# Kernel tuning notes

Measured on AMD Instinct MI355X. Metric: run time of the kernel, lower is better.

## Reference

```python
import jax, jax.numpy as jnp
import numpy as np
from jax import lax

A, T, B, OBS, H, ACT = 4, 128, 256, 128, 128, 8  # agents, time, envs, obs_dim, gru_hidden(=embed), act_dim


def setup_inputs() -> dict:
    key = jax.random.key(0)
    ks = jax.random.split(key, 16)
    def w(k, shape, fan_in):
        return (jax.random.normal(k, shape, jnp.float32) / np.float32(np.sqrt(fan_in)))
    return {
        "hstate": jnp.zeros((A, B, H), jnp.float32),
        "obs": jax.random.normal(ks[0], (A, T, B, OBS), jnp.float32),
        "avail_actions": jnp.ones((A, T, B, ACT), jnp.float32),
        # embedding dense
        "We": w(ks[1], (A, OBS, H), OBS), "be": jnp.zeros((A, H), jnp.float32),
        # GRU: input kernels (r|z|n concat) with bias, hidden kernels (r|z|n), only n-hidden has bias
        "Wi": w(ks[2], (A, H, 3 * H), H), "bi": jnp.zeros((A, 3 * H), jnp.float32),
        "Wh": w(ks[3], (A, H, 3 * H), H), "bhn": jnp.zeros((A, H), jnp.float32),
        # actor head
        "Wa1": w(ks[4], (A, H, H), H), "ba1": jnp.zeros((A, H), jnp.float32),
        "Wa2": 0.01 * w(ks[5], (A, H, ACT), H), "ba2": jnp.zeros((A, ACT), jnp.float32),
        "log_std": jnp.zeros((A, ACT), jnp.float32),
        # critic head
        "Wc1": w(ks[6], (A, H, H), H), "bc1": jnp.zeros((A, H), jnp.float32),
        "Wc2": w(ks[7], (A, H, 1), H), "bc2": jnp.zeros((A, 1), jnp.float32),
        "done": jax.random.bernoulli(ks[8], 0.05, (A, T, B)),
    }


def _agent_forward(h0, obs, done, avail_actions, We, be, Wi, bi, Wh, bhn,
                   Wa1, ba1, Wa2, ba2, log_std, Wc1, bc1, Wc2, bc2):
    # obs: [T,B,OBS], done: [T,B], h0: [B,H]
    act = jnp.tanh  # config['network']['activation'] == 'tanh'
    emb = act(jnp.einsum('tbo,oh->tbh', obs, We) + be)          # [T,B,H]
    xi = jnp.einsum('tbh,hg->tbg', emb, Wi) + bi                # [T,B,3H] precomputed input gates

    def step(h, xs):
        xi_t, d = xs                                            # [B,3H], [B]
        h = jnp.where(d[:, None], 0.0, h)                       # reset on done
        hh = h @ Wh                                             # [B,3H]
        xr, xz, xn = jnp.split(xi_t, 3, axis=-1)
        hr, hz, hn = jnp.split(hh, 3, axis=-1)
        r = jax.nn.sigmoid(xr + hr)
        z = jax.nn.sigmoid(xz + hz)
        n = jnp.tanh(xn + r * (hn + bhn))
        h_new = (1.0 - z) * n + z * h
        return h_new, h_new

    hT, ys = lax.scan(step, h0, (xi, done))                     # ys: [T,B,H]
    a = act(jnp.einsum('tbh,hk->tbk', ys, Wa1) + ba1)
    mean = jnp.einsum('tbh,ha->tba', a, Wa2) + ba2              # [T,B,ACT]
    std = jnp.exp(log_std)                                      # [ACT]
    c = act(jnp.einsum('tbh,hk->tbk', ys, Wc1) + bc1)
    value = (jnp.einsum('tbh,ho->tbo', c, Wc2) + bc2)[..., 0]   # [T,B]
    return hT, mean, std, value


def reference(hstate, obs, avail_actions, We, be, Wi, bi, Wh, bhn,
              Wa1, ba1, Wa2, ba2, log_std, Wc1, bc1, Wc2, bc2, done):
    hT, mean, std, value = jax.vmap(_agent_forward)(
        hstate, obs, done, avail_actions, We, be, Wi, bi, Wh, bhn,
        Wa1, ba1, Wa2, ba2, log_std, Wc1, bc1, Wc2, bc2)
    return hT, mean, std, value
```

## Files before the change

kernel.cpp:

```cpp
#include <hip/hip_runtime.h>

typedef unsigned short u16;
typedef __attribute__((ext_vector_type(8))) short short8;
typedef __attribute__((ext_vector_type(4))) float f32x4;

#define A_ 4
#define T_ 128
#define B_ 256
#define OBS_ 128
#define H_ 128
#define G_ 384
#define ACT_ 8
#define SIGS -1.4426950408889634f
#define TANS 2.8853900817779268f

__device__ __forceinline__ u16 f2b(float x) {
    unsigned int u = __float_as_uint(x);
    u = (u + 0x7fffu + ((u >> 16) & 1u)) >> 16;
    return (u16)u;
}
__device__ __forceinline__ u16 f2bc(float x) {
    return (u16)((__float_as_uint(x) + 0x8000u) >> 16);
}
__device__ __forceinline__ float b2f(u16 h) {
    return __uint_as_float(((unsigned int)h) << 16);
}
__device__ __forceinline__ float fexp2_(float x) { return __builtin_amdgcn_exp2f(x); }
__device__ __forceinline__ float frcp_(float x) { return __builtin_amdgcn_rcpf(x); }
__device__ __forceinline__ float sig_pre(float x) { return frcp_(1.0f + fexp2_(x)); }
__device__ __forceinline__ float tanh_pre(float x) {
    return fmaf(-2.0f, frcp_(1.0f + fexp2_(x)), 1.0f);
}
__device__ __forceinline__ f32x4 mfma16(short8 a, short8 b, f32x4 c) {
    return __builtin_amdgcn_mfma_f32_16x16x32_bf16(a, b, c, 0, 0, 0);
}

__global__ void k_prep(const float* __restrict__ We, const float* __restrict__ Wi,
                       const float* __restrict__ Wh, const float* __restrict__ Wa1,
                       const float* __restrict__ Wc1, const float* __restrict__ Wa2,
                       const float* __restrict__ Wc2, const float* __restrict__ log_std,
                       u16* __restrict__ weT, u16* __restrict__ wiT, u16* __restrict__ whT,
                       u16* __restrict__ wa1T, u16* __restrict__ wc1T, u16* __restrict__ h2T,
                       float* __restrict__ std_out) {
    const int PER_A = 149504;
    int idx = blockIdx.x * 256 + threadIdx.x;
    const int total = 4 * PER_A;
    if (idx < total) {
        int a = idx / PER_A;
        int i = idx % PER_A;
        if (i < 16384) {
            int h = i >> 7, o = i & 127;
            weT[a * 16384 + i] = f2b(TANS * We[a * 16384 + o * 128 + h]);
        } else if (i < 16384 + 49152) {
            int j = i - 16384; int g = j >> 7, k = j & 127;
            float s = (g < 256) ? SIGS : TANS;
            wiT[a * 49152 + j] = f2b(s * Wi[a * 49152 + k * 384 + g]);
        } else if (i < 16384 + 2 * 49152) {
            int j = i - 16384 - 49152; int g = j >> 7, k = j & 127;
            float s = (g < 256) ? SIGS : TANS;
            whT[a * 49152 + j] = f2b(s * Wh[a * 49152 + k * 384 + g]);
        } else if (i < 2 * 16384 + 2 * 49152) {
            int j = i - 16384 - 2 * 49152; int h2 = j >> 7, k = j & 127;
            wa1T[a * 16384 + j] = f2b(TANS * Wa1[a * 16384 + k * 128 + h2]);
        } else if (i < 3 * 16384 + 2 * 49152) {
            int j = i - 2 * 16384 - 2 * 49152; int h2 = j >> 7, k = j & 127;
            wc1T[a * 16384 + j] = f2b(TANS * Wc1[a * 16384 + k * 128 + h2]);
        } else {
            int j = i - 3 * 16384 - 2 * 49152; int row = j >> 7, k = j & 127;
            float v = 0.f;
            if (row < 8) v = Wa2[a * 1024 + k * 8 + row];
            else if (row == 8) v = Wc2[a * 128 + k];
            h2T[a * 2048 + j] = f2b(v);
        }
    } else if (idx < total + 32) {
        int i = idx - total;
        std_out[i] = __expf(log_std[i]);
    }
}

__global__ __launch_bounds__(512) void k_embed_xi(
    const float* __restrict__ obs, const float* __restrict__ be, const float* __restrict__ bi,
    const u16* __restrict__ weT, const u16* __restrict__ wiT, u16* __restrict__ xi_ws) {
    __shared__ __align__(16) u16 obsl[2][16][136];
    __shared__ __align__(16) u16 elds[2][16][136];
    const int a = blockIdx.y, t = blockIdx.x, half = blockIdx.z;
    const int wid = threadIdx.x >> 6, lane = threadIdx.x & 63;
    const int m = lane & 15, quad = lane >> 4;
    const int srow = threadIdx.x >> 5, schunk = threadIdx.x & 31;

    short8 we[4], wi[3][4];
    {
        const u16* p = weT + a * 16384 + (wid * 16 + m) * 128 + quad * 8;
#pragma unroll
        for (int ks = 0; ks < 4; ++ks) we[ks] = *(const short8*)(p + ks * 32);
#pragma unroll
        for (int g = 0; g < 3; ++g) {
            const u16* q = wiT + a * 49152 + (g * 128 + wid * 16 + m) * 128 + quad * 8;
#pragma unroll
            for (int ks = 0; ks < 4; ++ks) wi[g][ks] = *(const short8*)(q + ks * 32);
        }
    }
    const float bee = TANS * be[a * H_ + wid * 16 + m];
    float big[3];
#pragma unroll
    for (int g = 0; g < 3; ++g)
        big[g] = ((g < 2) ? SIGS : TANS) * bi[a * G_ + g * 128 + wid * 16 + m];

    const float* obsrow = obs + ((size_t)(a * T_ + t) * B_ + half * 128 + srow) * OBS_ + schunk * 4;
    ushort4* xi4 = (ushort4*)xi_ws;

    {
        float4 p0 = *(const float4*)(obsrow);
        ushort4 ob;
        ob.x = f2b(p0.x); ob.y = f2b(p0.y); ob.z = f2b(p0.z); ob.w = f2b(p0.w);
        *(ushort4*)&obsl[0][srow][schunk * 4] = ob;
    }
    float4 pf = *(const float4*)(obsrow + 2048);
    __syncthreads();

    for (int it = 0; it < 8; ++it) {
        short8 af[4];
#pragma unroll
        for (int ks = 0; ks < 4; ++ks)
            af[ks] = *(const short8*)&obsl[it & 1][m][ks * 32 + quad * 8];
        if (it + 1 < 8) {
            ushort4 ob;
            ob.x = f2b(pf.x); ob.y = f2b(pf.y); ob.z = f2b(pf.z); ob.w = f2b(pf.w);
            *(ushort4*)&obsl[(it + 1) & 1][srow][schunk * 4] = ob;
            if (it + 2 < 8) pf = *(const float4*)(obsrow + (size_t)(it + 2) * 2048);
        }

        f32x4 acc = f32x4{bee, bee, bee, bee};
#pragma unroll
        for (int ks = 0; ks < 4; ++ks) acc = mfma16(af[ks], we[ks], acc);
#pragma unroll
        for (int r = 0; r < 4; ++r)
            elds[it & 1][quad * 4 + r][wid * 16 + m] = f2bc(tanh_pre(acc[r]));

        if (it > 0) {
            short8 ef[4];
#pragma unroll
            for (int ks = 0; ks < 4; ++ks)
                ef[ks] = *(const short8*)&elds[(it - 1) & 1][m][ks * 32 + quad * 8];
            f32x4 xa[3];
#pragma unroll
            for (int g = 0; g < 3; ++g) xa[g] = f32x4{big[g], big[g], big[g], big[g]};
#pragma unroll
            for (int ks = 0; ks < 4; ++ks)
#pragma unroll
                for (int g = 0; g < 3; ++g) xa[g] = mfma16(ef[ks], wi[g][ks], xa[g]);
            const int itg = half * 8 + it - 1;
            const size_t base = ((size_t)(a * 16 + itg) * T_ + t) * 1536;
#pragma unroll
            for (int g = 0; g < 3; ++g) {
                ushort4 pk;
                pk.x = f2bc(xa[g][0]); pk.y = f2bc(xa[g][1]);
                pk.z = f2bc(xa[g][2]); pk.w = f2bc(xa[g][3]);
                xi4[base + (size_t)(wid * 3 + g) * 64 + lane] = pk;
            }
        }
        __syncthreads();
    }
    {
        short8 ef[4];
#pragma unroll
        for (int ks = 0; ks < 4; ++ks)
            ef[ks] = *(const short8*)&elds[1][m][ks * 32 + quad * 8];
        f32x4 xa[3];
#pragma unroll
        for (int g = 0; g < 3; ++g) xa[g] = f32x4{big[g], big[g], big[g], big[g]};
#pragma unroll
        for (int ks = 0; ks < 4; ++ks)
#pragma unroll
            for (int g = 0; g < 3; ++g) xa[g] = mfma16(ef[ks], wi[g][ks], xa[g]);
        const int itg = half * 8 + 7;
        const size_t base = ((size_t)(a * 16 + itg) * T_ + t) * 1536;
#pragma unroll
        for (int g = 0; g < 3; ++g) {
            ushort4 pk;
            pk.x = f2bc(xa[g][0]); pk.y = f2bc(xa[g][1]);
            pk.z = f2bc(xa[g][2]); pk.w = f2bc(xa[g][3]);
            xi4[base + (size_t)(wid * 3 + g) * 64 + lane] = pk;
        }
    }
}

__global__ __launch_bounds__(512, 2) void k_scan(
    const float* __restrict__ hstate, const u16* __restrict__ xi_ws,
    const u16* __restrict__ whT, const float* __restrict__ bhn,
    const int* __restrict__ done,
    const u16* __restrict__ wa1T, const u16* __restrict__ wc1T, const u16* __restrict__ h2T,
    const float* __restrict__ ba1, const float* __restrict__ bc1,
    const float* __restrict__ ba2, const float* __restrict__ bc2,
    float* __restrict__ hT_out, float* __restrict__ mean_out, float* __restrict__ val_out) {
    __shared__ __align__(16) u16 hlds[2][16][136];
    __shared__ __align__(16) u16 al[2][2][16][136];
    const int a = blockIdx.y, btile = blockIdx.x;
    const int wid = threadIdx.x >> 6, lane = threadIdx.x & 63;
    const int m = lane & 15, quad = lane >> 4;
    const int b0 = btile * 16;
    const int col = 16 * wid + m;

    short8 wh[3][4];
    const u16* whTa = whT + a * 49152;
#pragma unroll
    for (int g = 0; g < 3; ++g) {
        const u16* p = whTa + (g * 128 + col) * 128 + quad * 8;
#pragma unroll
        for (int ks = 0; ks < 4; ++ks) wh[g][ks] = *(const short8*)(p + ks * 32);
    }
    short8 wa[4], wc[4], h2f[4];
    {
        const u16* pa = wa1T + a * 16384 + col * 128 + quad * 8;
        const u16* pc = wc1T + a * 16384 + col * 128 + quad * 8;
        const u16* ph = h2T + a * 2048 + m * 128 + quad * 8;
#pragma unroll
        for (int ks = 0; ks < 4; ++ks) {
            wa[ks] = *(const short8*)(pa + ks * 32);
            wc[ks] = *(const short8*)(pc + ks * 32);
            h2f[ks] = *(const short8*)(ph + ks * 32);
        }
    }
    const float bh = TANS * bhn[a * H_ + col];
    const float fa = TANS * ba1[a * 128 + col];
    const float fc = TANS * bc1[a * 128 + col];
    float bb2 = 0.f;
    if (wid == 0) { if (m < 8) bb2 = ba2[a * 8 + m]; }
    else if (wid == 1) { if (m == 8) bb2 = bc2[a]; }

    float hm[4]; u16 hb[4];
#pragma unroll
    for (int r = 0; r < 4; ++r) {
        float v = hstate[((size_t)a * B_ + b0 + quad * 4 + r) * H_ + col];
        hm[r] = v; hb[r] = f2b(v);
    }

    const ushort4* xi4 = (const ushort4*)xi_ws;
    const size_t xibase = ((size_t)(a * 16 + btile) * T_) * 1536 + wid * 192 + lane;
    const int* dptr = done + (size_t)a * T_ * B_ + b0 + quad * 4;
    const int* dAq = done + (size_t)a * T_ * B_ + b0 + m;

    ushort4 px0 = xi4[xibase], px1 = xi4[xibase + 64], px2 = xi4[xibase + 128];
    int4 dn = *(const int4*)(dptr);
    int dead = dAq[0];

    for (int t = 0; t < T_; ++t) {
        u16 (*hl)[136] = hlds[t & 1];
#pragma unroll
        for (int r = 0; r < 4; ++r) hl[quad * 4 + r][col] = hb[r];
        if (dn.x) hm[0] = 0.f;
        if (dn.y) hm[1] = 0.f;
        if (dn.z) hm[2] = 0.f;
        if (dn.w) hm[3] = 0.f;
        __syncthreads();

        f32x4 ar, az, an;
        float xn[4];
        ar[0] = b2f(px0.x); ar[1] = b2f(px0.y); ar[2] = b2f(px0.z); ar[3] = b2f(px0.w);
        az[0] = b2f(px1.x); az[1] = b2f(px1.y); az[2] = b2f(px1.z); az[3] = b2f(px1.w);
        xn[0] = b2f(px2.x); xn[1] = b2f(px2.y); xn[2] = b2f(px2.z); xn[3] = b2f(px2.w);
        an = f32x4{bh, bh, bh, bh};
        const int deadcur = dead;
        if (t + 1 < T_) {
            const size_t nx = xibase + (size_t)(t + 1) * 1536;
            px0 = xi4[nx]; px1 = xi4[nx + 64]; px2 = xi4[nx + 128];
            dn = *(const int4*)(dptr + (size_t)(t + 1) * B_);
            dead = dAq[(size_t)(t + 1) * B_];
        }

        short8 af[4];
#pragma unroll
        for (int ks = 0; ks < 4; ++ks)
            af[ks] = *(const short8*)&hl[m][ks * 32 + quad * 8];

        f32x4 aa, ac;
        if (t > 0) {
            aa = f32x4{fa, fa, fa, fa};
            ac = f32x4{fc, fc, fc, fc};
#pragma unroll
            for (int ks = 0; ks < 4; ++ks) {
                aa = mfma16(af[ks], wa[ks], aa);
                ac = mfma16(af[ks], wc[ks], ac);
            }
        }

        short8 afr[4];
#pragma unroll
        for (int ks = 0; ks < 4; ++ks) afr[ks] = af[ks];
        if (__any(deadcur)) {
            const short8 z8 = short8{0, 0, 0, 0, 0, 0, 0, 0};
#pragma unroll
            for (int ks = 0; ks < 4; ++ks) if (deadcur) afr[ks] = z8;
        }
#pragma unroll
        for (int ks = 0; ks < 4; ++ks) {
            ar = mfma16(afr[ks], wh[0][ks], ar);
            az = mfma16(afr[ks], wh[1][ks], az);
            an = mfma16(afr[ks], wh[2][ks], an);
        }

        if (t > 0) {
#pragma unroll
            for (int r = 0; r < 4; ++r) {
                al[t & 1][0][quad * 4 + r][col] = f2bc(tanh_pre(aa[r]));
                al[t & 1][1][quad * 4 + r][col] = f2bc(tanh_pre(ac[r]));
            }
        }

#pragma unroll
        for (int r = 0; r < 4; ++r) {
            const float rg = sig_pre(ar[r]);
            const float zg = sig_pre(az[r]);
            const float ng = tanh_pre(fmaf(rg, an[r], xn[r]));
            const float hn2 = fmaf(zg, hm[r] - ng, ng);
            hm[r] = hn2;
            hb[r] = f2bc(hn2);
        }

        if (t >= 2 && wid < 2) {
            short8 tf[4];
#pragma unroll
            for (int ks = 0; ks < 4; ++ks)
                tf[ks] = *(const short8*)&al[(t - 1) & 1][wid][m][ks * 32 + quad * 8];
            f32x4 tacc = f32x4{bb2, bb2, bb2, bb2};
#pragma unroll
            for (int ks = 0; ks < 4; ++ks) tacc = mfma16(tf[ks], h2f[ks], tacc);
            const size_t R0 = (size_t)a * 32768 + (size_t)(t - 2) * 256 + b0;
            if (wid == 0) {
                if (m < 8) {
#pragma unroll
                    for (int r = 0; r < 4; ++r)
                        mean_out[(R0 + quad * 4 + r) * 8 + m] = tacc[r];
                }
            } else {
                if (m == 8) {
#pragma unroll
                    for (int r = 0; r < 4; ++r)
                        val_out[R0 + quad * 4 + r] = tacc[r];
                }
            }
        }
    }

#pragma unroll
    for (int r = 0; r < 4; ++r)
        hT_out[((size_t)a * B_ + b0 + quad * 4 + r) * H_ + col] = hm[r];

    {
        u16 (*hl)[136] = hlds[0];
#pragma unroll
        for (int r = 0; r < 4; ++r) hl[quad * 4 + r][col] = hb[r];
        __syncthreads();
        short8 af[4];
#pragma unroll
        for (int ks = 0; ks < 4; ++ks)
            af[ks] = *(const short8*)&hl[m][ks * 32 + quad * 8];
        f32x4 aa = f32x4{fa, fa, fa, fa};
        f32x4 ac = f32x4{fc, fc, fc, fc};
#pragma unroll
        for (int ks = 0; ks < 4; ++ks) {
            aa = mfma16(af[ks], wa[ks], aa);
            ac = mfma16(af[ks], wc[ks], ac);
        }
#pragma unroll
        for (int r = 0; r < 4; ++r) {
            al[0][0][quad * 4 + r][col] = f2bc(tanh_pre(aa[r]));
            al[0][1][quad * 4 + r][col] = f2bc(tanh_pre(ac[r]));
        }
        if (wid < 2) {
            short8 tf[4];
#pragma unroll
            for (int ks = 0; ks < 4; ++ks)
                tf[ks] = *(const short8*)&al[1][wid][m][ks * 32 + quad * 8];
            f32x4 tacc = f32x4{bb2, bb2, bb2, bb2};
#pragma unroll
            for (int ks = 0; ks < 4; ++ks) tacc = mfma16(tf[ks], h2f[ks], tacc);
            const size_t R0 = (size_t)a * 32768 + (size_t)(T_ - 2) * 256 + b0;
            if (wid == 0) {
                if (m < 8) {
#pragma unroll
                    for (int r = 0; r < 4; ++r)
                        mean_out[(R0 + quad * 4 + r) * 8 + m] = tacc[r];
                }
            } else {
                if (m == 8) {
#pragma unroll
                    for (int r = 0; r < 4; ++r)
                        val_out[R0 + quad * 4 + r] = tacc[r];
                }
            }
        }
        __syncthreads();
        if (wid < 2) {
            short8 tf[4];
#pragma unroll
            for (int ks = 0; ks < 4; ++ks)
                tf[ks] = *(const short8*)&al[0][wid][m][ks * 32 + quad * 8];
            f32x4 tacc = f32x4{bb2, bb2, bb2, bb2};
#pragma unroll
            for (int ks = 0; ks < 4; ++ks) tacc = mfma16(tf[ks], h2f[ks], tacc);
            const size_t R0 = (size_t)a * 32768 + (size_t)(T_ - 1) * 256 + b0;
            if (wid == 0) {
                if (m < 8) {
#pragma unroll
                    for (int r = 0; r < 4; ++r)
                        mean_out[(R0 + quad * 4 + r) * 8 + m] = tacc[r];
                }
            } else {
                if (m == 8) {
#pragma unroll
                    for (int r = 0; r < 4; ++r)
                        val_out[R0 + quad * 4 + r] = tacc[r];
                }
            }
        }
    }
}

extern "C" void kernel_launch(void* const* d_in, const int* in_sizes, int n_in,
                              void* d_out, int out_size, void* d_ws, size_t ws_size,
                              hipStream_t stream) {
    const float* hstate = (const float*)d_in[0];
    const float* obs = (const float*)d_in[1];
    const float* We = (const float*)d_in[3];
    const float* be = (const float*)d_in[4];
    const float* Wi = (const float*)d_in[5];
    const float* bi = (const float*)d_in[6];
    const float* Wh = (const float*)d_in[7];
    const float* bhn = (const float*)d_in[8];
    const float* Wa1 = (const float*)d_in[9];
    const float* ba1 = (const float*)d_in[10];
    const float* Wa2 = (const float*)d_in[11];
    const float* ba2 = (const float*)d_in[12];
    const float* log_std = (const float*)d_in[13];
    const float* Wc1 = (const float*)d_in[14];
    const float* bc1 = (const float*)d_in[15];
    const float* Wc2 = (const float*)d_in[16];
    const float* bc2 = (const float*)d_in[17];
    const int* done = (const int*)d_in[18];

    float* out = (float*)d_out;
    float* hT_out = out;
    float* mean_out = out + 131072;
    float* std_out = out + 1179648;
    float* val_out = out + 1179680;

    u16* ws = (u16*)d_ws;
    u16* xi = ws;
    u16* ys = xi + 50331648;
    u16* weT = ys + 16777216;
    u16* wiT = weT + 65536;
    u16* whT = wiT + 196608;
    u16* wa1T = whT + 196608;
    u16* wc1T = wa1T + 65536;
    u16* h2T = wc1T + 65536;

    hipLaunchKernelGGL(k_prep, dim3(2337), dim3(256), 0, stream,
                       We, Wi, Wh, Wa1, Wc1, Wa2, Wc2, log_std,
                       weT, wiT, whT, wa1T, wc1T, h2T, std_out);
    hipLaunchKernelGGL(k_embed_xi, dim3(128, 4, 2), dim3(512), 0, stream,
                       obs, be, bi, weT, wiT, xi);
    hipLaunchKernelGGL(k_scan, dim3(16, 4), dim3(512), 0, stream,
                       hstate, xi, whT, bhn, done,
                       wa1T, wc1T, h2T, ba1, bc1, ba2, bc2,
                       hT_out, mean_out, val_out);
}
```

Before: 302.7 us.

## Fuse embedding and input-gate projection into the recurrent scan kernel

Drops the separate embed/xi kernel and its large bf16 workspace round-trip. The scan kernel now loads obs per timestep, computes the embedding with MFMA one step ahead, and adds the input-gate MFMAs into the gate accumulators. This removes a global write and read of the precomputed gates, but adds per-step MFMA work and register pressure to the serial recurrent loop, which has only 64 blocks.

```diff
diff --git a/kernel.cpp b/kernel.cpp
--- a/kernel.cpp
+++ b/kernel.cpp
@@ -21,9 +21,6 @@
 }
 __device__ __forceinline__ u16 f2bc(float x) {
     return (u16)((__float_as_uint(x) + 0x8000u) >> 16);
-}
-__device__ __forceinline__ float b2f(u16 h) {
-    return __uint_as_float(((unsigned int)h) << 16);
 }
 __device__ __forceinline__ float fexp2_(float x) { return __builtin_amdgcn_exp2f(x); }
 __device__ __forceinline__ float frcp_(float x) { return __builtin_amdgcn_rcpf(x); }
@@ -78,139 +75,45 @@
     }
 }
 
-__global__ __launch_bounds__(512) void k_embed_xi(
-    const float* __restrict__ obs, const float* __restrict__ be, const float* __restrict__ bi,
-    const u16* __restrict__ weT, const u16* __restrict__ wiT, u16* __restrict__ xi_ws) {
-    __shared__ __align__(16) u16 obsl[2][16][136];
-    __shared__ __align__(16) u16 elds[2][16][136];
-    const int a = blockIdx.y, t = blockIdx.x, half = blockIdx.z;
-    const int wid = threadIdx.x >> 6, lane = threadIdx.x & 63;
-    const int m = lane & 15, quad = lane >> 4;
-    const int srow = threadIdx.x >> 5, schunk = threadIdx.x & 31;
-
-    short8 we[4], wi[3][4];
-    {
-        const u16* p = weT + a * 16384 + (wid * 16 + m) * 128 + quad * 8;
-#pragma unroll
-        for (int ks = 0; ks < 4; ++ks) we[ks] = *(const short8*)(p + ks * 32);
-#pragma unroll
-        for (int g = 0; g < 3; ++g) {
-            const u16* q = wiT + a * 49152 + (g * 128 + wid * 16 + m) * 128 + quad * 8;
-#pragma unroll
-            for (int ks = 0; ks < 4; ++ks) wi[g][ks] = *(const short8*)(q + ks * 32);
-        }
-    }
-    const float bee = TANS * be[a * H_ + wid * 16 + m];
-    float big[3];
-#pragma unroll
-    for (int g = 0; g < 3; ++g)
-        big[g] = ((g < 2) ? SIGS : TANS) * bi[a * G_ + g * 128 + wid * 16 + m];
-
-    const float* obsrow = obs + ((size_t)(a * T_ + t) * B_ + half * 128 + srow) * OBS_ + schunk * 4;
-    ushort4* xi4 = (ushort4*)xi_ws;
-
-    {
-        float4 p0 = *(const float4*)(obsrow);
-        ushort4 ob;
-        ob.x = f2b(p0.x); ob.y = f2b(p0.y); ob.z = f2b(p0.z); ob.w = f2b(p0.w);
-        *(ushort4*)&obsl[0][srow][schunk * 4] = ob;
-    }
-    float4 pf = *(const float4*)(obsrow + 2048);
-    __syncthreads();
-
-    for (int it = 0; it < 8; ++it) {
-        short8 af[4];
-#pragma unroll
-        for (int ks = 0; ks < 4; ++ks)
-            af[ks] = *(const short8*)&obsl[it & 1][m][ks * 32 + quad * 8];
-        if (it + 1 < 8) {
-            ushort4 ob;
-            ob.x = f2b(pf.x); ob.y = f2b(pf.y); ob.z = f2b(pf.z); ob.w = f2b(pf.w);
-            *(ushort4*)&obsl[(it + 1) & 1][srow][schunk * 4] = ob;
-            if (it + 2 < 8) pf = *(const float4*)(obsrow + (size_t)(it + 2) * 2048);
-        }
-
-        f32x4 acc = f32x4{bee, bee, bee, bee};
-#pragma unroll
-        for (int ks = 0; ks < 4; ++ks) acc = mfma16(af[ks], we[ks], acc);
-#pragma unroll
-        for (int r = 0; r < 4; ++r)
-            elds[it & 1][quad * 4 + r][wid * 16 + m] = f2bc(tanh_pre(acc[r]));
-
-        if (it > 0) {
-            short8 ef[4];
-#pragma unroll
-            for (int ks = 0; ks < 4; ++ks)
-                ef[ks] = *(const short8*)&elds[(it - 1) & 1][m][ks * 32 + quad * 8];
-            f32x4 xa[3];
-#pragma unroll
-            for (int g = 0; g < 3; ++g) xa[g] = f32x4{big[g], big[g], big[g], big[g]};
-#pragma unroll
-            for (int ks = 0; ks < 4; ++ks)
-#pragma unroll
-                for (int g = 0; g < 3; ++g) xa[g] = mfma16(ef[ks], wi[g][ks], xa[g]);
-            const int itg = half * 8 + it - 1;
-            const size_t base = ((size_t)(a * 16 + itg) * T_ + t) * 1536;
-#pragma unroll
-            for (int g = 0; g < 3; ++g) {
-                ushort4 pk;
-                pk.x = f2bc(xa[g][0]); pk.y = f2bc(xa[g][1]);
-                pk.z = f2bc(xa[g][2]); pk.w = f2bc(xa[g][3]);
-                xi4[base + (size_t)(wid * 3 + g) * 64 + lane] = pk;
-            }
-        }
-        __syncthreads();
-    }
-    {
-        short8 ef[4];
-#pragma unroll
-        for (int ks = 0; ks < 4; ++ks)
-            ef[ks] = *(const short8*)&elds[1][m][ks * 32 + quad * 8];
-        f32x4 xa[3];
-#pragma unroll
-        for (int g = 0; g < 3; ++g) xa[g] = f32x4{big[g], big[g], big[g], big[g]};
-#pragma unroll
-        for (int ks = 0; ks < 4; ++ks)
-#pragma unroll
-            for (int g = 0; g < 3; ++g) xa[g] = mfma16(ef[ks], wi[g][ks], xa[g]);
-        const int itg = half * 8 + 7;
-        const size_t base = ((size_t)(a * 16 + itg) * T_ + t) * 1536;
-#pragma unroll
-        for (int g = 0; g < 3; ++g) {
-            ushort4 pk;
-            pk.x = f2bc(xa[g][0]); pk.y = f2bc(xa[g][1]);
-            pk.z = f2bc(xa[g][2]); pk.w = f2bc(xa[g][3]);
-            xi4[base + (size_t)(wid * 3 + g) * 64 + lane] = pk;
-        }
-    }
-}
-
 __global__ __launch_bounds__(512, 2) void k_scan(
-    const float* __restrict__ hstate, const u16* __restrict__ xi_ws,
-    const u16* __restrict__ whT, const float* __restrict__ bhn,
-    const int* __restrict__ done,
+    const float* __restrict__ hstate, const float* __restrict__ obs,
+    const u16* __restrict__ weT, const u16* __restrict__ wiT,
+    const u16* __restrict__ whT,
+    const float* __restrict__ be, const float* __restrict__ bi,
+    const float* __restrict__ bhn, const int* __restrict__ done,
     const u16* __restrict__ wa1T, const u16* __restrict__ wc1T, const u16* __restrict__ h2T,
     const float* __restrict__ ba1, const float* __restrict__ bc1,
     const float* __restrict__ ba2, const float* __restrict__ bc2,
     float* __restrict__ hT_out, float* __restrict__ mean_out, float* __restrict__ val_out) {
     __shared__ __align__(16) u16 hlds[2][16][136];
+    __shared__ __align__(16) u16 obsl[2][16][136];
+    __shared__ __align__(16) u16 elds[2][16][136];
     __shared__ __align__(16) u16 al[2][2][16][136];
     const int a = blockIdx.y, btile = blockIdx.x;
     const int wid = threadIdx.x >> 6, lane = threadIdx.x & 63;
     const int m = lane & 15, quad = lane >> 4;
     const int b0 = btile * 16;
     const int col = 16 * wid + m;
-
-    short8 wh[3][4];
-    const u16* whTa = whT + a * 49152;
-#pragma unroll
-    for (int g = 0; g < 3; ++g) {
-        const u16* p = whTa + (g * 128 + col) * 128 + quad * 8;
-#pragma unroll
-        for (int ks = 0; ks < 4; ++ks) wh[g][ks] = *(const short8*)(p + ks * 32);
-    }
-    short8 wa[4], wc[4], h2f[4];
+    const int srow = threadIdx.x >> 5, schunk = threadIdx.x & 31;
+
+    short8 wh[3][4], we[4], wi[3][4], wa[4], wc[4], h2f[4];
     {
+        const u16* whTa = whT + a * 49152;
+#pragma unroll
+        for (int g = 0; g < 3; ++g) {
+            const u16* p = whTa + (g * 128 + col) * 128 + quad * 8;
+#pragma unroll
+            for (int ks = 0; ks < 4; ++ks) wh[g][ks] = *(const short8*)(p + ks * 32);
+        }
+        const u16* pe = weT + a * 16384 + col * 128 + quad * 8;
+#pragma unroll
+        for (int ks = 0; ks < 4; ++ks) we[ks] = *(const short8*)(pe + ks * 32);
+#pragma unroll
+        for (int g = 0; g < 3; ++g) {
+            const u16* q = wiT + a * 49152 + (g * 128 + col) * 128 + quad * 8;
+#pragma unroll
+            for (int ks = 0; ks < 4; ++ks) wi[g][ks] = *(const short8*)(q + ks * 32);
+        }
         const u16* pa = wa1T + a * 16384 + col * 128 + quad * 8;
         const u16* pc = wc1T + a * 16384 + col * 128 + quad * 8;
         const u16* ph = h2T + a * 2048 + m * 128 + quad * 8;
@@ -222,6 +125,10 @@
         }
     }
     const float bh = TANS * bhn[a * H_ + col];
+    const float bee = TANS * be[a * H_ + col];
+    const float bir = SIGS * bi[a * G_ + col];
+    const float biz = SIGS * bi[a * G_ + 128 + col];
+    const float bin = TANS * bi[a * G_ + 256 + col];
     const float fa = TANS * ba1[a * 128 + col];
     const float fc = TANS * bc1[a * 128 + col];
     float bb2 = 0.f;
@@ -235,14 +142,33 @@
         hm[r] = v; hb[r] = f2b(v);
     }
 
-    const ushort4* xi4 = (const ushort4*)xi_ws;
-    const size_t xibase = ((size_t)(a * 16 + btile) * T_) * 1536 + wid * 192 + lane;
     const int* dptr = done + (size_t)a * T_ * B_ + b0 + quad * 4;
     const int* dAq = done + (size_t)a * T_ * B_ + b0 + m;
-
-    ushort4 px0 = xi4[xibase], px1 = xi4[xibase + 64], px2 = xi4[xibase + 128];
     int4 dn = *(const int4*)(dptr);
     int dead = dAq[0];
+
+    const float* obsrow = obs + ((size_t)a * T_ * B_ + b0 + srow) * OBS_ + schunk * 4;
+
+    {
+        float4 p0 = *(const float4*)(obsrow);
+        ushort4 ob;
+        ob.x = f2b(p0.x); ob.y = f2b(p0.y); ob.z = f2b(p0.z); ob.w = f2b(p0.w);
+        *(ushort4*)&obsl[0][srow][schunk * 4] = ob;
+    }
+    float4 pf = *(const float4*)(obsrow + (size_t)B_ * OBS_);
+    __syncthreads();
+    {
+        short8 of[4];
+#pragma unroll
+        for (int ks = 0; ks < 4; ++ks)
+            of[ks] = *(const short8*)&obsl[0][m][ks * 32 + quad * 8];
+        f32x4 eacc = f32x4{bee, bee, bee, bee};
+#pragma unroll
+        for (int ks = 0; ks < 4; ++ks) eacc = mfma16(of[ks], we[ks], eacc);
+#pragma unroll
+        for (int r = 0; r < 4; ++r)
+            elds[0][quad * 4 + r][col] = f2bc(tanh_pre(eacc[r]));
+    }
 
     for (int t = 0; t < T_; ++t) {
         u16 (*hl)[136] = hlds[t & 1];
@@ -252,26 +178,26 @@
         if (dn.y) hm[1] = 0.f;
         if (dn.z) hm[2] = 0.f;
         if (dn.w) hm[3] = 0.f;
+        if (t + 1 < T_) {
+            ushort4 ob;
+            ob.x = f2b(pf.x); ob.y = f2b(pf.y); ob.z = f2b(pf.z); ob.w = f2b(pf.w);
+            *(ushort4*)&obsl[(t + 1) & 1][srow][schunk * 4] = ob;
+        }
         __syncthreads();
 
-        f32x4 ar, az, an;
-        float xn[4];
-        ar[0] = b2f(px0.x); ar[1] = b2f(px0.y); ar[2] = b2f(px0.z); ar[3] = b2f(px0.w);
-        az[0] = b2f(px1.x); az[1] = b2f(px1.y); az[2] = b2f(px1.z); az[3] = b2f(px1.w);
-        xn[0] = b2f(px2.x); xn[1] = b2f(px2.y); xn[2] = b2f(px2.z); xn[3] = b2f(px2.w);
-        an = f32x4{bh, bh, bh, bh};
         const int deadcur = dead;
+        if (t + 2 < T_) pf = *(const float4*)(obsrow + (size_t)(t + 2) * B_ * OBS_);
         if (t + 1 < T_) {
-            const size_t nx = xibase + (size_t)(t + 1) * 1536;
-            px0 = xi4[nx]; px1 = xi4[nx + 64]; px2 = xi4[nx + 128];
             dn = *(const int4*)(dptr + (size_t)(t + 1) * B_);
             dead = dAq[(size_t)(t + 1) * B_];
         }
 
-        short8 af[4];
-#pragma unroll
-        for (int ks = 0; ks < 4; ++ks)
+        short8 af[4], ef[4];
+#pragma unroll
+        for (int ks = 0; ks < 4; ++ks) {
             af[ks] = *(const short8*)&hl[m][ks * 32 + quad * 8];
+            ef[ks] = *(const short8*)&elds[t & 1][m][ks * 32 + quad * 8];
+        }
 
         f32x4 aa, ac;
         if (t > 0) {
@@ -283,20 +209,40 @@
                 ac = mfma16(af[ks], wc[ks], ac);
             }
         }
-
-        short8 afr[4];
-#pragma unroll
-        for (int ks = 0; ks < 4; ++ks) afr[ks] = af[ks];
         if (__any(deadcur)) {
             const short8 z8 = short8{0, 0, 0, 0, 0, 0, 0, 0};
 #pragma unroll
-            for (int ks = 0; ks < 4; ++ks) if (deadcur) afr[ks] = z8;
-        }
+            for (int ks = 0; ks < 4; ++ks) if (deadcur) af[ks] = z8;
+        }
+
+        f32x4 ar = f32x4{bir, bir, bir, bir};
+        f32x4 az = f32x4{biz, biz, biz, biz};
+        f32x4 xn = f32x4{bin, bin, bin, bin};
+        f32x4 an = f32x4{bh, bh, bh, bh};
 #pragma unroll
         for (int ks = 0; ks < 4; ++ks) {
-            ar = mfma16(afr[ks], wh[0][ks], ar);
-            az = mfma16(afr[ks], wh[1][ks], az);
-            an = mfma16(afr[ks], wh[2][ks], an);
+            ar = mfma16(ef[ks], wi[0][ks], ar);
+            az = mfma16(ef[ks], wi[1][ks], az);
+            xn = mfma16(ef[ks], wi[2][ks], xn);
+            an = mfma16(af[ks], wh[2][ks], an);
+        }
+#pragma unroll
+        for (int ks = 0; ks < 4; ++ks) {
+            ar = mfma16(af[ks], wh[0][ks], ar);
+            az = mfma16(af[ks], wh[1][ks], az);
+        }
+
+        if (t + 1 < T_) {
+            short8 of[4];
+#pragma unroll
+            for (int ks = 0; ks < 4; ++ks)
+                of[ks] = *(const short8*)&obsl[(t + 1) & 1][m][ks * 32 + quad * 8];
+            f32x4 eacc = f32x4{bee, bee, bee, bee};
+#pragma unroll
+            for (int ks = 0; ks < 4; ++ks) eacc = mfma16(of[ks], we[ks], eacc);
+#pragma unroll
+            for (int r = 0; r < 4; ++r)
+                elds[(t + 1) & 1][quad * 4 + r][col] = f2bc(tanh_pre(eacc[r]));
         }
 
         if (t > 0) {
@@ -458,10 +404,8 @@
     hipLaunchKernelGGL(k_prep, dim3(2337), dim3(256), 0, stream,
                        We, Wi, Wh, Wa1, Wc1, Wa2, Wc2, log_std,
                        weT, wiT, whT, wa1T, wc1T, h2T, std_out);
-    hipLaunchKernelGGL(k_embed_xi, dim3(128, 4, 2), dim3(512), 0, stream,
-                       obs, be, bi, weT, wiT, xi);
     hipLaunchKernelGGL(k_scan, dim3(16, 4), dim3(512), 0, stream,
-                       hstate, xi, whT, bhn, done,
+                       hstate, obs, weT, wiT, whT, be, bi, bhn, done,
                        wa1T, wc1T, h2T, ba1, bc1, ba2, bc2,
                        hT_out, mean_out, val_out);
 }
```

Result: slower. 414.5 us (+37.0%).
